# Optimization experiments

Hardware: AMD Instinct MI355X
Metric: run time of the kernel (lower is better)

The kernel has to match this reference:

```python
import jax, jax.numpy as jnp
import numpy as np

N_NODES = 50000


def setup_inputs() -> dict:
    key = jax.random.key(0)
    ks = jax.random.split(key, 9)
    x = jax.random.normal(ks[0], (N_NODES, 32), dtype=jnp.float32)
    pos = jax.random.normal(ks[1], (N_NODES, 3), dtype=jnp.float32)
    edge_index = jax.random.randint(ks[2], (2, 1600000), 0, N_NODES, dtype=jnp.int64)
    W1 = jax.random.normal(ks[3], (35, 64), dtype=jnp.float32) * 0.1
    b1 = jnp.zeros((64,), dtype=jnp.float32)
    W2 = jax.random.normal(ks[4], (64, 64), dtype=jnp.float32) * 0.1
    b2 = jnp.zeros((64,), dtype=jnp.float32)
    Wg = jax.random.normal(ks[5], (64, 128), dtype=jnp.float32) * 0.1
    bg = jnp.zeros((128,), dtype=jnp.float32)
    return {"x": x, "pos": pos, "edge_index": edge_index,
            "W1": W1, "b1": b1, "W2": W2, "b2": b2, "Wg": Wg, "bg": bg}


def reference(x, pos, edge_index, W1, b1, W2, b2, Wg, bg):
    N = x.shape[0]
    # add_self_loops=True: append (i, i) edges
    self_idx = jnp.arange(N, dtype=edge_index.dtype)
    src = jnp.concatenate([edge_index[0], self_idx])  # message source j
    dst = jnp.concatenate([edge_index[1], self_idx])  # aggregation target i
    # message: concat(x_j, pos_j - pos_i) -> local_nn (Lin+ReLU x2)
    msg = jnp.concatenate([x[src], pos[src] - pos[dst]], axis=-1)  # [E+N, 35]
    h = jax.nn.relu(msg @ W1 + b1)  # [E+N, 64]
    h = jax.nn.relu(h @ W2 + b2)    # [E+N, 64]
    # max aggregation per destination node (self loops guarantee nonempty segments)
    agg = jax.ops.segment_max(h, dst, num_segments=N)  # [N, 64]
    # global_nn: Linear
    return agg @ Wg + bg  # [N, 128]
```

## Files before the change

### kernel.cpp

```cpp
#include <hip/hip_runtime.h>

#define N_NODES 50000
#define N_EDGES 1600000
#define N_TOTAL (N_EDGES + N_NODES)
#define F_IN    32
#define HID     64
#define F_OUT   128
#define G       32
#define NB      1563
#define NBIN    392
#define CAP1_MAX 5120
#define OVF_CAP 16384
#define W1WIN   4096
#define NNODEBLK 196

#define OFF_QBF   0
#define OFF_CUR1  (N_NODES * 32)
#define OFF_OVFC  (OFF_CUR1 + NBIN * 16)
#define OFF_CELLB (OFF_OVFC + 16)
#define OFF_CELLC (OFF_CELLB + NB)
#define OFF_OVF   (OFF_CELLC + NB + 2)
#define OFF_BIN   (OFF_OVF + OVF_CAP)
#define NCLR      (NBIN * 16 + 16)

typedef __attribute__((ext_vector_type(2))) _Float16 h2f;
typedef __attribute__((ext_vector_type(8))) _Float16 half8;
typedef __attribute__((ext_vector_type(4))) float v4f;

__device__ __forceinline__ unsigned f2h2(float a, float b) {
    h2f v;
    v.x = (_Float16)a; v.y = (_Float16)b;
    return __builtin_bit_cast(unsigned, v);
}

__device__ __forceinline__ unsigned hsubmax0(unsigned a, unsigned b) {
    h2f x = __builtin_bit_cast(h2f, a) - __builtin_bit_cast(h2f, b);
    h2f z = {(_Float16)0.f, (_Float16)0.f};
    x = __builtin_elementwise_max(x, z);
    return __builtin_bit_cast(unsigned, x);
}

__device__ __forceinline__ float h2lo(unsigned u) { return (float)__builtin_bit_cast(h2f, u).x; }
__device__ __forceinline__ float h2hi(unsigned u) { return (float)__builtin_bit_cast(h2f, u).y; }
__device__ __forceinline__ float f16r(float x)    { return (float)(_Float16)x; }

#define WAVE_FENCE() do { asm volatile("s_waitcnt lgkmcnt(0)" ::: "memory"); \
                          __builtin_amdgcn_sched_barrier(0); } while (0)

__global__ __launch_bounds__(256) void zero_kernel(unsigned* __restrict__ clr)
{
    const int i = blockIdx.x * 256 + threadIdx.x;
    if (i < NCLR) clr[i] = 0u;
}

__global__ __launch_bounds__(1024) void bin_kernel(
    const int* __restrict__ ei, unsigned* __restrict__ cur1,
    unsigned* __restrict__ bin1, unsigned* __restrict__ ovfc,
    unsigned* __restrict__ ovf, int cap1)
{
    __shared__ unsigned stage[W1WIN];
    __shared__ unsigned binid[W1WIN];
    __shared__ unsigned hist[NBIN], startp[NBIN + 1], gbase[NBIN];
    __shared__ unsigned wpart[16];

    const int t = threadIdx.x;
    const int wbase = blockIdx.x * W1WIN;

    for (int i = t; i < NBIN; i += 1024) hist[i] = 0u;
    __syncthreads();

    unsigned ev[4]; int bv[4]; unsigned rv[4]; bool val[4];
    #pragma unroll
    for (int k = 0; k < 4; ++k) {
        const int idx = wbase + k * 1024 + t;
        val[k] = idx < N_TOTAL;
        if (val[k]) {
            int s, d;
            if (idx < N_EDGES) { s = ei[idx]; d = ei[N_EDGES + idx]; }
            else               { s = d = idx - N_EDGES; }
            ev[k] = ((unsigned)d << 16) | (unsigned)s;
            bv[k] = d >> 7;
            rv[k] = atomicAdd(&hist[bv[k]], 1u);
        }
    }
    __syncthreads();

    unsigned hv = 0;
    if (t < NBIN) hv = hist[t];
    unsigned v = hv;
    #pragma unroll
    for (int o = 1; o < 64; o <<= 1) {
        const unsigned u = __shfl_up(v, o, 64);
        if ((t & 63) >= o) v += u;
    }
    if ((t & 63) == 63) wpart[t >> 6] = v;
    __syncthreads();
    if (t == 0) {
        unsigned r = 0;
        #pragma unroll
        for (int i = 0; i < 16; ++i) { const unsigned c2 = wpart[i]; wpart[i] = r; r += c2; }
        startp[NBIN] = r;
    }
    __syncthreads();
    if (t < NBIN) startp[t] = (v - hv) + wpart[t >> 6];
    if (t < NBIN && hv) gbase[t] = atomicAdd(&cur1[t * 16], hv);
    __syncthreads();

    #pragma unroll
    for (int k = 0; k < 4; ++k)
        if (val[k]) {
            const unsigned pos = startp[bv[k]] + rv[k];
            stage[pos] = ev[k]; binid[pos] = (unsigned)bv[k];
        }
    __syncthreads();

    const unsigned total = startp[NBIN];
    for (unsigned i = t; i < total; i += 1024u) {
        const unsigned b = binid[i];
        const unsigned gp = gbase[b] + (i - startp[b]);
        if (gp < (unsigned)cap1) bin1[b * (unsigned)cap1 + gp] = stage[i];
        else {
            const unsigned qo = atomicAdd(ovfc, 1u);
            if (qo < OVF_CAP) ovf[qo] = stage[i];
        }
    }
}

__global__ __launch_bounds__(1024) void refine_pre_kernel(
    unsigned* __restrict__ bin1, const unsigned* __restrict__ cur1,
    unsigned* __restrict__ cellbase, unsigned* __restrict__ cellcnt, int cap1,
    const float* __restrict__ x, const float* __restrict__ pos,
    const float* __restrict__ W1, const float* __restrict__ b1,
    unsigned* __restrict__ qbf)
{
    __shared__ unsigned ebuf[CAP1_MAX];
    __shared__ unsigned ebuf2[CAP1_MAX];
    __shared__ unsigned cnt32[4 * 32];
    __shared__ unsigned startp[5];
    __shared__ unsigned ssum;
    __shared__ float    w1s[35 * HID + HID];

    const int t = threadIdx.x;

    if (blockIdx.x >= NBIN) {
        for (int i = t; i < 35 * HID; i += 1024) w1s[i] = W1[i];
        if (t < HID) w1s[35 * HID + t] = b1[t];
        __syncthreads();

        const int n = (blockIdx.x - NBIN) * 256 + (t >> 2);
        const int sub = t & 3;
        const int lane = t & 63;
        if (n >= N_NODES) return;

        const float4* x4 = (const float4*)(x + (long long)n * F_IN);
        const float4 xa = x4[sub * 2], xb = x4[sub * 2 + 1];
        const float xv[8] = {xa.x, xa.y, xa.z, xa.w, xb.x, xb.y, xb.z, xb.w};

        float acc[16];
        #pragma unroll
        for (int k = 0; k < 16; ++k) acc[k] = w1s[35 * HID + sub * 16 + k];

        #pragma unroll
        for (int c = 0; c < F_IN; ++c) {
            const float xm = __shfl(xv[c & 7], (lane & 60) | (c >> 3), 64);
            #pragma unroll
            for (int k = 0; k < 16; ++k)
                acc[k] = fmaf(xm, w1s[c * HID + sub * 16 + k], acc[k]);
        }
        #pragma unroll
        for (int a = 0; a < 3; ++a) {
            const float pp = pos[n * 3 + a];
            #pragma unroll
            for (int k = 0; k < 16; ++k)
                acc[k] = fmaf(pp, w1s[(F_IN + a) * HID + sub * 16 + k], acc[k]);
        }

        uint4* o4 = (uint4*)(qbf + (unsigned)n * 32u + (unsigned)sub * 8u);
        o4[0] = make_uint4(f2h2(acc[0], acc[1]),  f2h2(acc[2], acc[3]),
                           f2h2(acc[4], acc[5]),  f2h2(acc[6], acc[7]));
        o4[1] = make_uint4(f2h2(acc[8], acc[9]),  f2h2(acc[10], acc[11]),
                           f2h2(acc[12], acc[13]), f2h2(acc[14], acc[15]));
        return;
    }

    const int bb = blockIdx.x;
    const unsigned n1 = min(cur1[bb * 16], (unsigned)cap1);
    const unsigned base1 = (unsigned)bb * (unsigned)cap1;
    const int rep = t & 31, lane = t & 63;

    if (t < 128) cnt32[t] = 0u;
    __syncthreads();

    for (unsigned i = t; i < n1; i += 1024u) {
        const unsigned e = bin1[base1 + i];
        ebuf[i] = e;
        atomicAdd(&cnt32[(((e >> 21) & 3u) << 5) + rep], 1u);
    }
    __syncthreads();

    unsigned ow = 0;
    if (t < 128) ow = cnt32[t];
    unsigned v = ow;
    #pragma unroll
    for (int o = 1; o < 64; o <<= 1) {
        const unsigned u = __shfl_up(v, o, 64);
        if (lane >= o) v += u;
    }
    if (t == 63) ssum = v;
    __syncthreads();
    if (t >= 64 && t < 128) v += ssum;
    if (t < 128) {
        cnt32[t] = v - ow;
        if ((t & 31) == 0) startp[t >> 5] = v - ow;
    }
    if (t == 0) startp[4] = n1;
    __syncthreads();

    if (t < 4) {
        const int cell = bb * 4 + t;
        if (cell < NB) {
            cellbase[cell] = base1 + startp[t];
            cellcnt[cell]  = startp[t + 1] - startp[t];
        }
    }

    for (unsigned i = t; i < n1; i += 1024u) {
        const unsigned e = ebuf[i];
        const unsigned p = atomicAdd(&cnt32[(((e >> 21) & 3u) << 5) + rep], 1u);
        ebuf2[p] = (((e >> 16) & 31u) << 16) | (e & 0xFFFFu);
    }
    __syncthreads();
    for (unsigned i = t; i < n1; i += 1024u) bin1[base1 + i] = ebuf2[i];
}

__global__ __launch_bounds__(256, 4) void gather_kernel(
    const unsigned* __restrict__ qbf,
    const float* __restrict__ pos,
    const unsigned* __restrict__ cellbase,
    const unsigned* __restrict__ cellcnt,
    const unsigned* __restrict__ bkt,
    const float* __restrict__ W1p,
    const float* __restrict__ W2, const float* __restrict__ b2,
    float* __restrict__ out)
{
    __shared__ unsigned aggs[(G + 1) * HID];
    __shared__ unsigned w2t[64 * 32];
    __shared__ unsigned rlds[G * 32];
    __shared__ unsigned ast[4][64 * 16];

    const int t = threadIdx.x, lane = t & 63, w = t >> 6;
    const int q = lane >> 4, m15 = lane & 15;
    const int b = blockIdx.x;
    const unsigned cnt  = cellcnt[b];
    const unsigned base = cellbase[b];

    for (int i = t; i < (G + 1) * HID; i += 256) aggs[i] = 0u;
    for (int i = t; i < 64 * 32; i += 256) {
        const int nn = i >> 5, ku = i & 31;
        w2t[(nn << 5) + ((((ku >> 2) ^ (nn & 7)) << 2) | (ku & 3))] =
            f2h2(W2[(2 * ku) * HID + nn], W2[(2 * ku + 1) * HID + nn]);
    }
    for (int i = t; i < G * 32; i += 256) {
        const int dl = i >> 5, k2 = i & 31;
        const int node = b * G + dl;
        float v0 = 0.f, v1 = 0.f;
        if (node < N_NODES) {
            #pragma unroll
            for (int a = 0; a < 3; ++a) {
                const float pp = pos[node * 3 + a];
                v0 = fmaf(pp, W1p[a * HID + 2 * k2], v0);
                v1 = fmaf(pp, W1p[a * HID + 2 * k2 + 1], v1);
            }
        }
        rlds[(dl << 5) + ((((k2 >> 2) ^ (dl & 7)) << 2) | (k2 & 3))] = f2h2(v0, v1);
    }
    __syncthreads();

    float b2v[4];
    #pragma unroll
    for (int nt = 0; nt < 4; ++nt) b2v[nt] = b2[nt * 16 + m15];

    unsigned* aw = ast[w];
    const int axw = ((lane >> 1) & 3) << 2;
    const int axr = ((m15 >> 1) & 3) << 2;
    const unsigned nit = (cnt + 255u) >> 8;

    #pragma unroll 1
    for (unsigned it = 0; it < nit; ++it) {
        const unsigned off = it * 256u + (unsigned)w * 64u;
        const unsigned rem = (off < cnt) ? min(64u, cnt - off) : 0u;
        const unsigned f = off + (unsigned)lane;
        unsigned pent = 0u;
        if (f < cnt) pent = bkt[base + f];
        const int s = (int)(pent & 0xFFFFu), dl = (int)(pent >> 16);

        const uint4* qr = (const uint4*)(qbf + (unsigned)s * 32u);
        uint4 qv[8];
        #pragma unroll
        for (int i = 0; i < 8; ++i) qv[i] = qr[i];

        const int rbase = dl << 5, rx = dl & 7;

        half8 a0[4], a1[4];
        #pragma unroll
        for (int hf = 0; hf < 2; ++hf) {
            #pragma unroll
            for (int j4 = 0; j4 < 4; ++j4) {
                const uint4 r4 = *(const uint4*)(
                    rlds + rbase + (((hf * 4 + j4) ^ rx) << 2));
                const uint4 qq = qv[hf * 4 + j4];
                uint4 hh;
                hh.x = hsubmax0(qq.x, r4.x);
                hh.y = hsubmax0(qq.y, r4.y);
                hh.z = hsubmax0(qq.z, r4.z);
                hh.w = hsubmax0(qq.w, r4.w);
                *(uint4*)(aw + (lane << 4) + ((j4 << 2) ^ axw)) = hh;
            }
            WAVE_FENCE();
            half8* af = hf ? a1 : a0;
            #pragma unroll
            for (int mt = 0; mt < 4; ++mt)
                af[mt] = *(const half8*)(
                    aw + ((mt * 16 + m15) << 4) + ((q << 2) ^ axr));
            WAVE_FENCE();
        }

        int dsh[16];
        #pragma unroll
        for (int i = 0; i < 16; ++i) {
            const int er = (i >> 2) * 16 + q * 4 + (i & 3);
            const int dv = __shfl(dl, er, 64);
            const int dle = ((unsigned)er < rem) ? dv : G;
            dsh[i] = (dle << 6) + m15;
        }

        #pragma unroll
        for (int h = 0; h < 2; ++h) {
            half8 bf[2][2];
            const int nx = m15 & 7;
            #pragma unroll
            for (int ntl = 0; ntl < 2; ++ntl) {
                const int nn = (2 * h + ntl) * 16 + m15;
                #pragma unroll
                for (int ks = 0; ks < 2; ++ks)
                    bf[ntl][ks] = *(const half8*)(
                        w2t + (nn << 5) + (((ks * 4 + q) ^ nx) << 2));
            }
            v4f c[4][2];
            #pragma unroll
            for (int mt = 0; mt < 4; ++mt)
                #pragma unroll
                for (int ntl = 0; ntl < 2; ++ntl) {
                    const float bb2 = b2v[2 * h + ntl];
                    c[mt][ntl] = (v4f){bb2, bb2, bb2, bb2};
                }
            #pragma unroll
            for (int mt = 0; mt < 4; ++mt)
                #pragma unroll
                for (int ntl = 0; ntl < 2; ++ntl) {
                    c[mt][ntl] = __builtin_amdgcn_mfma_f32_16x16x32_f16(
                        a0[mt], bf[ntl][0], c[mt][ntl], 0, 0, 0);
                    c[mt][ntl] = __builtin_amdgcn_mfma_f32_16x16x32_f16(
                        a1[mt], bf[ntl][1], c[mt][ntl], 0, 0, 0);
                }
            #pragma unroll
            for (int mt = 0; mt < 4; ++mt)
                #pragma unroll
                for (int r = 0; r < 4; ++r) {
                    const int ab = dsh[mt * 4 + r];
                    #pragma unroll
                    for (int ntl = 0; ntl < 2; ++ntl) {
                        const float hv = fmaxf(c[mt][ntl][r], 0.f);
                        atomicMax(&aggs[ab + (2 * h + ntl) * 16],
                                  __float_as_uint(hv));
                    }
                }
        }
    }

    __syncthreads();
    for (int i = t; i < G * HID; i += 256) {
        const int row = i >> 6, ch = i & 63, n = b * G + row;
        if (n < N_NODES)
            out[(long long)n * F_OUT + HID + ch] = __uint_as_float(aggs[i]);
    }
}

__global__ __launch_bounds__(64) void ovf_kernel(
    const unsigned* __restrict__ qbf, const float* __restrict__ pos,
    const unsigned* __restrict__ ovfc, const unsigned* __restrict__ ovf,
    const float* __restrict__ W1p, const float* __restrict__ W2,
    const float* __restrict__ b2, unsigned* __restrict__ aggbits)
{
    const unsigned n = min(*ovfc, (unsigned)OVF_CAP);
    for (unsigned i = blockIdx.x * 64 + threadIdx.x; i < n; i += gridDim.x * 64) {
        const unsigned p = ovf[i];
        const int s = (int)(p & 0xFFFFu), d = (int)(p >> 16);
        float h1[HID];
        #pragma unroll 1
        for (int k = 0; k < HID; ++k) {
            const unsigned u = qbf[s * 32 + (k >> 1)];
            const float qp = (k & 1) ? h2hi(u) : h2lo(u);
            float r = 0.f;
            #pragma unroll 1
            for (int a = 0; a < 3; ++a) r = fmaf(pos[d * 3 + a], W1p[a * HID + k], r);
            h1[k] = fmaxf(f16r(qp - f16r(r)), 0.f);
        }
        unsigned* ap = aggbits + (long long)d * F_OUT + HID;
        #pragma unroll 1
        for (int k = 0; k < HID; ++k) {
            float a2 = b2[k];
            #pragma unroll 1
            for (int j = 0; j < HID; ++j)
                a2 = fmaf(h1[j], f16r(W2[j * HID + k]), a2);
            a2 = fmaxf(a2, 0.f);
            atomicMax(ap + k, __float_as_uint(a2));
        }
    }
}

__global__ __launch_bounds__(256) void out_gemm_kernel(
    float* __restrict__ out,
    const float* __restrict__ Wg,
    const float* __restrict__ bg)
{
    const int lane = threadIdx.x & 63;
    const int wave = blockIdx.x * (blockDim.x >> 6) + (threadIdx.x >> 6);
    const int nwav = gridDim.x * (blockDim.x >> 6);

    float w1r[HID], w2r[HID];
    #pragma unroll
    for (int j = 0; j < HID; ++j) {
        w1r[j] = Wg[j * F_OUT + lane];
        w2r[j] = Wg[j * F_OUT + 64 + lane];
    }
    const float bga = bg[lane];
    const float bgb = bg[64 + lane];

    for (int n = wave; n < N_NODES; n += nwav) {
        float* row = out + (long long)n * F_OUT;
        const float a = row[64 + lane];
        float y1 = bga, y2 = bgb;
        #pragma unroll
        for (int j = 0; j < HID; ++j) {
            const float aj = __shfl(a, j, 64);
            y1 = fmaf(aj, w1r[j], y1);
            y2 = fmaf(aj, w2r[j], y2);
        }
        row[lane]      = y1;
        row[64 + lane] = y2;
    }
}

extern "C" void kernel_launch(void* const* d_in, const int* in_sizes, int n_in,
                              void* d_out, int out_size, void* d_ws, size_t ws_size,
                              hipStream_t stream) {
    const float* x   = (const float*)d_in[0];
    const float* pos = (const float*)d_in[1];
    const int*   ei  = (const int*)d_in[2];
    const float* W1  = (const float*)d_in[3];
    const float* b1  = (const float*)d_in[4];
    const float* W2  = (const float*)d_in[5];
    const float* b2  = (const float*)d_in[6];
    const float* Wg  = (const float*)d_in[7];
    const float* bg  = (const float*)d_in[8];
    float* out = (float*)d_out;

    unsigned* ws    = (unsigned*)d_ws;
    unsigned* qbf   = ws + OFF_QBF;
    unsigned* cur1  = ws + OFF_CUR1;
    unsigned* ovfc  = ws + OFF_OVFC;
    unsigned* cellb = ws + OFF_CELLB;
    unsigned* cellc = ws + OFF_CELLC;
    unsigned* ovf   = ws + OFF_OVF;
    unsigned* bin1  = ws + OFF_BIN;

    long long avail = (long long)(ws_size / 4) - OFF_BIN;
    int cap1 = (int)(avail / NBIN);
    if (cap1 > CAP1_MAX) cap1 = CAP1_MAX;
    if (cap1 < 2048) cap1 = 2048;

    zero_kernel<<<(NCLR + 255) / 256, 256, 0, stream>>>(cur1);
    bin_kernel<<<(N_TOTAL + W1WIN - 1) / W1WIN, 1024, 0, stream>>>(
        ei, cur1, bin1, ovfc, ovf, cap1);
    refine_pre_kernel<<<NBIN + NNODEBLK, 1024, 0, stream>>>(
        bin1, cur1, cellb, cellc, cap1, x, pos, W1, b1, qbf);
    gather_kernel<<<NB, 256, 0, stream>>>(
        qbf, pos, cellb, cellc, bin1, W1 + F_IN * HID, W2, b2, out);
    ovf_kernel<<<32, 64, 0, stream>>>(
        qbf, pos, ovfc, ovf, W1 + F_IN * HID, W2, b2, (unsigned*)out);
    out_gemm_kernel<<<512, 256, 0, stream>>>(out, Wg, bg);
}
```

Measured before the change: 220.1 us.

## Keep W2 MFMA fragments in registers and drop redundant LDS arrays

In the gather kernel, W2 B-fragments are now loaded once into registers per thread, replacing the shared-memory w2t table that was re-read every iteration. This cuts LDS use and per-iteration LDS reads, and the launch bound is raised to 5 blocks per SM to exploit the freed LDS. In the bin kernel, the separate binid shared array is removed and the bin id is recovered from the packed entry's high bits. Holding 16 extra VGPRs of fragments under a tighter register budget risks spills.

```diff
diff --git a/kernel.cpp b/kernel.cpp
--- a/kernel.cpp
+++ b/kernel.cpp
@@ -59,7 +59,6 @@
     unsigned* __restrict__ ovf, int cap1)
 {
     __shared__ unsigned stage[W1WIN];
-    __shared__ unsigned binid[W1WIN];
     __shared__ unsigned hist[NBIN], startp[NBIN + 1], gbase[NBIN];
     __shared__ unsigned wpart[16];
 
@@ -108,20 +107,18 @@
 
     #pragma unroll
     for (int k = 0; k < 4; ++k)
-        if (val[k]) {
-            const unsigned pos = startp[bv[k]] + rv[k];
-            stage[pos] = ev[k]; binid[pos] = (unsigned)bv[k];
-        }
+        if (val[k]) stage[startp[bv[k]] + rv[k]] = ev[k];
     __syncthreads();
 
     const unsigned total = startp[NBIN];
     for (unsigned i = t; i < total; i += 1024u) {
-        const unsigned b = binid[i];
+        const unsigned e = stage[i];
+        const unsigned b = e >> 23;
         const unsigned gp = gbase[b] + (i - startp[b]);
-        if (gp < (unsigned)cap1) bin1[b * (unsigned)cap1 + gp] = stage[i];
+        if (gp < (unsigned)cap1) bin1[b * (unsigned)cap1 + gp] = e;
         else {
             const unsigned qo = atomicAdd(ovfc, 1u);
-            if (qo < OVF_CAP) ovf[qo] = stage[i];
+            if (qo < OVF_CAP) ovf[qo] = e;
         }
     }
 }
@@ -233,7 +230,7 @@
     for (unsigned i = t; i < n1; i += 1024u) bin1[base1 + i] = ebuf2[i];
 }
 
-__global__ __launch_bounds__(256, 4) void gather_kernel(
+__global__ __launch_bounds__(256, 5) void gather_kernel(
     const unsigned* __restrict__ qbf,
     const float* __restrict__ pos,
     const unsigned* __restrict__ cellbase,
@@ -244,7 +241,6 @@
     float* __restrict__ out)
 {
     __shared__ unsigned aggs[(G + 1) * HID];
-    __shared__ unsigned w2t[64 * 32];
     __shared__ unsigned rlds[G * 32];
     __shared__ unsigned ast[4][64 * 16];
 
@@ -255,11 +251,6 @@
     const unsigned base = cellbase[b];
 
     for (int i = t; i < (G + 1) * HID; i += 256) aggs[i] = 0u;
-    for (int i = t; i < 64 * 32; i += 256) {
-        const int nn = i >> 5, ku = i & 31;
-        w2t[(nn << 5) + ((((ku >> 2) ^ (nn & 7)) << 2) | (ku & 3))] =
-            f2h2(W2[(2 * ku) * HID + nn], W2[(2 * ku + 1) * HID + nn]);
-    }
     for (int i = t; i < G * 32; i += 256) {
         const int dl = i >> 5, k2 = i & 31;
         const int node = b * G + dl;
@@ -274,11 +265,29 @@
         }
         rlds[(dl << 5) + ((((k2 >> 2) ^ (dl & 7)) << 2) | (k2 & 3))] = f2h2(v0, v1);
     }
-    __syncthreads();
-
+
+    half8 bfr[2][2][2];
+    #pragma unroll
+    for (int h = 0; h < 2; ++h)
+        #pragma unroll
+        for (int ntl = 0; ntl < 2; ++ntl) {
+            const int nn = (2 * h + ntl) * 16 + m15;
+            #pragma unroll
+            for (int ks = 0; ks < 2; ++ks) {
+                half8 vv;
+                #pragma unroll
+                for (int j = 0; j < 4; ++j) {
+                    const int ku = (ks * 4 + q) * 4 + j;
+                    vv[2 * j]     = (_Float16)W2[(2 * ku) * HID + nn];
+                    vv[2 * j + 1] = (_Float16)W2[(2 * ku + 1) * HID + nn];
+                }
+                bfr[h][ntl][ks] = vv;
+            }
+        }
     float b2v[4];
     #pragma unroll
     for (int nt = 0; nt < 4; ++nt) b2v[nt] = b2[nt * 16 + m15];
+    __syncthreads();
 
     unsigned* aw = ast[w];
     const int axw = ((lane >> 1) & 3) << 2;
@@ -336,16 +345,6 @@
 
         #pragma unroll
         for (int h = 0; h < 2; ++h) {
-            half8 bf[2][2];
-            const int nx = m15 & 7;
-            #pragma unroll
-            for (int ntl = 0; ntl < 2; ++ntl) {
-                const int nn = (2 * h + ntl) * 16 + m15;
-                #pragma unroll
-                for (int ks = 0; ks < 2; ++ks)
-                    bf[ntl][ks] = *(const half8*)(
-                        w2t + (nn << 5) + (((ks * 4 + q) ^ nx) << 2));
-            }
             v4f c[4][2];
             #pragma unroll
             for (int mt = 0; mt < 4; ++mt)
@@ -359,9 +358,9 @@
                 #pragma unroll
                 for (int ntl = 0; ntl < 2; ++ntl) {
                     c[mt][ntl] = __builtin_amdgcn_mfma_f32_16x16x32_f16(
-                        a0[mt], bf[ntl][0], c[mt][ntl], 0, 0, 0);
+                        a0[mt], bfr[h][ntl][0], c[mt][ntl], 0, 0, 0);
                     c[mt][ntl] = __builtin_amdgcn_mfma_f32_16x16x32_f16(
-                        a1[mt], bf[ntl][1], c[mt][ntl], 0, 0, 0);
+                        a1[mt], bfr[h][ntl][1], c[mt][ntl], 0, 0, 0);
                 }
             #pragma unroll
             for (int mt = 0; mt < 4; ++mt)
```

After: 419.2 us. 90.5% more time.
